# Kernel tuning notes

Hardware: AMD Instinct MI355X
Metric: run time of the kernel (lower is better)

The kernel has to match this reference:

```python
import jax, jax.numpy as jnp
import numpy as np

B, T, D, F = 32, 512, 512, 256
K = 3
MEL_MAX = 4096
EPS = 1e-5


def _xavier(key, shape, fan_in, fan_out):
    lim = float(np.sqrt(6.0 / (fan_in + fan_out)))
    return jax.random.uniform(key, shape, jnp.float32, -lim, lim)


def setup_inputs() -> dict:
    key = jax.random.key(0)
    ks = jax.random.split(key, 6)
    x = jax.random.normal(ks[0], (B, T, D), jnp.float32)
    target = jax.random.randint(ks[1], (B, T), 0, 8)  # per-token durations
    # conv weights stored as [K, I, O] (lax 'WIO'); torch xavier on [O,I,K]: fan_in=I*K, fan_out=O*K
    w1 = _xavier(ks[2], (K, D, F), D * K, F * K)
    b1 = jnp.zeros((F,), jnp.float32)
    g1 = jnp.ones((F,), jnp.float32)
    be1 = jnp.zeros((F,), jnp.float32)
    w2 = _xavier(ks[3], (K, F, F), F * K, F * K)
    b2 = jnp.zeros((F,), jnp.float32)
    g2 = jnp.ones((F,), jnp.float32)
    be2 = jnp.zeros((F,), jnp.float32)
    wl = _xavier(ks[4], (F, 1), F, 1)
    bl = jnp.zeros((1,), jnp.float32)
    return dict(x=x, target=target, mel_max_length=MEL_MAX,
                w1=w1, b1=b1, g1=g1, be1=be1,
                w2=w2, b2=b2, g2=g2, be2=be2, wl=wl, bl=bl)


def _layer_norm(h, g, b):
    mu = jnp.mean(h, axis=-1, keepdims=True)
    var = jnp.mean(jnp.square(h - mu), axis=-1, keepdims=True)
    return (h - mu) * jax.lax.rsqrt(var + EPS) * g + b


def _conv1d(h, w, b):
    # h: [B,T,C_in], w: [K,C_in,C_out]; torch padding=1 with K=3 == SAME
    out = jax.lax.conv_general_dilated(h, w, (1,), 'SAME',
                                       dimension_numbers=('NWC', 'WIO', 'NWC'))
    return out + b


def reference(x, target, mel_max_length, w1, b1, g1, be1, w2, b2, g2, be2, wl, bl):
    # ---- DurationPredictor (eval: dropout = identity) ----
    h = jax.nn.relu(_layer_norm(_conv1d(x, w1, b1), g1, be1))
    h = jax.nn.relu(_layer_norm(_conv1d(h, w2, b2), g2, be2))
    dur_pred = jax.nn.relu(h @ wl + bl)[..., 0]  # [B, T]

    # ---- LR: ragged expansion of x by `target` durations, padded to mel_max_length ----
    cum = jnp.cumsum(target, axis=1)              # [B, T]
    total = cum[:, -1]                            # [B]
    pos = jnp.arange(mel_max_length)              # [M]
    # frame m maps to token i with cum[i-1] <= m < cum[i]
    idx = jax.vmap(lambda c: jnp.searchsorted(c, pos, side='right'))(cum)  # [B, M]
    idx = jnp.clip(idx, 0, x.shape[1] - 1)
    mask = pos[None, :] < total[:, None]          # [B, M]
    out = jnp.take_along_axis(x, idx[..., None], axis=1) * mask[..., None].astype(x.dtype)
    return (out, dur_pred)
```

## Files before the change

### kernel.cpp

```cpp
#include <hip/hip_runtime.h>
#include <type_traits>

#define B_   32
#define T_   512
#define D_   512
#define F_   256
#define MEL  4096
#define EPS_ 1e-5f

typedef __attribute__((ext_vector_type(8))) short bf16x8;
typedef __attribute__((ext_vector_type(4))) float f32x4;

#define GLL16(gp, lp) \
    __builtin_amdgcn_global_load_lds((const __attribute__((address_space(1))) void*)(gp), \
                                     (__attribute__((address_space(3))) void*)(lp), 16, 0, 0)
#define BARRIER() do { asm volatile("" ::: "memory"); __builtin_amdgcn_s_barrier(); \
                       asm volatile("" ::: "memory"); } while (0)

__device__ inline unsigned short f2bf(float f) {
    unsigned u = __float_as_uint(f);
    unsigned r = (u + 0x7fff + ((u >> 16) & 1)) >> 16;
    return (unsigned short)r;
}

__global__ void prep_w_kernel(const float* __restrict__ w1, const float* __restrict__ w2,
                              unsigned short* __restrict__ w1T, unsigned short* __restrict__ w2T)
{
    int idx = blockIdx.x * 256 + threadIdx.x;
    if (idx < 3 * D_ * F_) {
        int kk = idx / F_, f = idx % F_;
        w1T[(size_t)f * (3 * D_) + kk] = f2bf(w1[idx]);
    } else {
        int j = idx - 3 * D_ * F_;
        if (j < 3 * F_ * F_) {
            int kk = j / F_, f = j % F_;
            w2T[(size_t)f * (3 * F_) + kk] = f2bf(w2[j]);
        }
    }
}

template<int IN_D, typename InT, bool FUSE_DUR>
__global__ __launch_bounds__(512, 1)
void conv_mfma_kernel(const InT* __restrict__ x, const unsigned short* __restrict__ wT,
                      const float* __restrict__ bias, const float* __restrict__ gamma,
                      const float* __restrict__ beta, unsigned short* __restrict__ out,
                      const float* __restrict__ wl, const float* __restrict__ bl,
                      float* __restrict__ dur)
{
    constexpr int MT = 64;
    constexpr int KT = 3 * IN_D;
    constexpr int PHASES = KT / 64;

    __shared__ __align__(16) char xs_raw[(MT + 2) * IN_D * 2];
    __shared__ __align__(16) unsigned short xsB[2 * 16384];
    __shared__ float red[MT][8];
    __shared__ float redD[MT][4];

    const int blocksPerBatch = T_ / MT;
    const int b  = blockIdx.x / blocksPerBatch;
    const int t0 = (blockIdx.x % blocksPerBatch) * MT;
    const int l  = threadIdx.x & 63;
    const int wv = threadIdx.x >> 6;
    const int fg = wv & 3;
    const int rg = wv >> 2;

    constexpr int CH = (MT + 2) * IN_D / 8;
    for (int c = threadIdx.x; c < CH; c += 512) {
        int j  = c / (IN_D / 8);
        int d8 = (c % (IN_D / 8)) * 8;
        int t  = t0 - 1 + j;
        uint4 pk = make_uint4(0u, 0u, 0u, 0u);
        if (t >= 0 && t < T_) {
            if constexpr (std::is_same_v<InT, float>) {
                const float4* src = reinterpret_cast<const float4*>(&x[((size_t)b * T_ + t) * IN_D + d8]);
                float4 a0 = src[0], a1 = src[1];
                pk.x = (unsigned)f2bf(a0.x) | ((unsigned)f2bf(a0.y) << 16);
                pk.y = (unsigned)f2bf(a0.z) | ((unsigned)f2bf(a0.w) << 16);
                pk.z = (unsigned)f2bf(a1.x) | ((unsigned)f2bf(a1.y) << 16);
                pk.w = (unsigned)f2bf(a1.z) | ((unsigned)f2bf(a1.w) << 16);
            } else {
                pk = *reinterpret_cast<const uint4*>(&x[((size_t)b * T_ + t) * IN_D + d8]);
            }
        }
        int byte = ((j * IN_D + d8) * 2) ^ ((j & 7) << 4);
        *reinterpret_cast<uint4*>(&xs_raw[byte]) = pk;
    }

    float bv[4], gv[4], bev[4], wlv[4];
#pragma unroll
    for (int n = 0; n < 4; ++n) {
        int f = fg * 64 + n * 16 + (l & 15);
        bv[n] = bias[f]; gv[n] = gamma[f]; bev[n] = beta[f];
        if constexpr (FUSE_DUR) wlv[n] = wl[f];
    }
    float blv = FUSE_DUR ? bl[0] : 0.f;

    __syncthreads();

    const int sbase = wv * 4;
    auto stageB = [&](int ph, int buf) {
        int p = ph < PHASES ? ph : PHASES - 1;
        unsigned short* lb = &xsB[buf * 16384];
#pragma unroll
        for (int i = 0; i < 4; ++i) {
            int s = sbase + i;
            int c = s * 64 + l;
            int f = c >> 3;
            int kg = (c & 7) ^ (f & 7);
            const unsigned short* src = wT + (size_t)f * KT + p * 64 + kg * 8;
            GLL16(src, lb + s * 512);
        }
    };

    auto loadBfrag = [&](bf16x8* dst, int buf, int kk2) {
#pragma unroll
        for (int n = 0; n < 4; ++n) {
            int f  = fg * 64 + n * 16 + (l & 15);
            int kg = kk2 * 4 + (l >> 4);
            dst[n] = *reinterpret_cast<const bf16x8*>(&xsB[buf * 16384 + f * 64 + ((kg ^ (f & 7)) * 8)]);
        }
    };
    const int k_lane = (l >> 4) * 8;
    auto loadA = [&](bf16x8* dst, int kk) {
        int kp = kk / IN_D;
        int dbase = (kk % IN_D) + k_lane;
#pragma unroll
        for (int m = 0; m < 2; ++m) {
            int j = rg * 32 + m * 16 + (l & 15) + kp;
            int byte = ((j * IN_D + dbase) * 2) ^ ((j & 7) << 4);
            dst[m] = *reinterpret_cast<const bf16x8*>(&xs_raw[byte]);
        }
    };

    f32x4 acc[2][4];
#pragma unroll
    for (int m = 0; m < 2; ++m)
#pragma unroll
        for (int n = 0; n < 4; ++n) acc[m][n] = (f32x4){0.f, 0.f, 0.f, 0.f};

    stageB(0, 0);
    stageB(1, 1);
    for (int p = 0; p < PHASES; ++p) {
        asm volatile("s_waitcnt vmcnt(4)" ::: "memory");
        BARRIER();
        int buf = p & 1;
#pragma unroll
        for (int kk2 = 0; kk2 < 2; ++kk2) {
            int kk = p * 64 + kk2 * 32;
            bf16x8 Bv[4], Av[2];
            loadBfrag(Bv, buf, kk2);
            loadA(Av, kk);
#pragma unroll
            for (int m = 0; m < 2; ++m)
#pragma unroll
                for (int n = 0; n < 4; ++n)
                    acc[m][n] = __builtin_amdgcn_mfma_f32_16x16x32_bf16(Av[m], Bv[n], acc[m][n], 0, 0, 0);
        }
        BARRIER();
        stageB(p + 2, buf);
    }

#pragma unroll
    for (int m = 0; m < 2; ++m)
#pragma unroll
        for (int q = 0; q < 4; ++q) {
            float s = 0.f, s2 = 0.f;
#pragma unroll
            for (int n = 0; n < 4; ++n) {
                float v = acc[m][n][q] + bv[n];
                acc[m][n][q] = v;
                s += v; s2 += v * v;
            }
#pragma unroll
            for (int o = 1; o < 16; o <<= 1) { s += __shfl_xor(s, o); s2 += __shfl_xor(s2, o); }
            int row = rg * 32 + m * 16 + (l >> 4) * 4 + q;
            if ((l & 15) == 0) { red[row][fg * 2] = s; red[row][fg * 2 + 1] = s2; }
        }
    __syncthreads();

#pragma unroll
    for (int m = 0; m < 2; ++m)
#pragma unroll
        for (int q = 0; q < 4; ++q) {
            int row = rg * 32 + m * 16 + (l >> 4) * 4 + q;
            float s  = red[row][0] + red[row][2] + red[row][4] + red[row][6];
            float s2 = red[row][1] + red[row][3] + red[row][5] + red[row][7];
            float mu  = s * (1.f / F_);
            float var = s2 * (1.f / F_) - mu * mu;
            float rs  = rsqrtf(var + EPS_);
            size_t rbase = ((size_t)(b * T_ + t0 + row)) * F_;
            float part = 0.f;
#pragma unroll
            for (int n = 0; n < 4; ++n) {
                float y = (acc[m][n][q] - mu) * rs * gv[n] + bev[n];
                y = fmaxf(y, 0.f);
                out[rbase + fg * 64 + n * 16 + (l & 15)] = f2bf(y);
                if constexpr (FUSE_DUR) part = fmaf(y, wlv[n], part);
            }
            if constexpr (FUSE_DUR) {
#pragma unroll
                for (int o = 1; o < 16; o <<= 1) part += __shfl_xor(part, o);
                if ((l & 15) == 0) redD[row][fg] = part;
            }
        }

    if constexpr (FUSE_DUR) {
        __syncthreads();
        if (threadIdx.x < MT) {
            float s = redD[threadIdx.x][0] + redD[threadIdx.x][1]
                    + redD[threadIdx.x][2] + redD[threadIdx.x][3] + blv;
            dur[(size_t)b * T_ + t0 + threadIdx.x] = fmaxf(s, 0.f);
        }
    }
}

__global__ __launch_bounds__(256)
void cumsum_kernel(const int* __restrict__ tgt, int* __restrict__ cum)
{
    int b = blockIdx.x;
    int tid = threadIdx.x;
    int t0 = tid * 2;
    int a0 = tgt[b * T_ + t0], a1 = tgt[b * T_ + t0 + 1];
    int lane = tid & 63, w = tid >> 6;
    int v = a0 + a1;
#pragma unroll
    for (int o = 1; o < 64; o <<= 1) { int u = __shfl_up(v, o); if (lane >= o) v += u; }
    __shared__ int wsum[4];
    if (lane == 63) wsum[w] = v;
    __syncthreads();
    int base = 0;
#pragma unroll
    for (int i = 0; i < 4; ++i) if (i < w) base += wsum[i];
    int incl = base + v;
    cum[b * T_ + t0]     = incl - a1;
    cum[b * T_ + t0 + 1] = incl;
}

__global__ __launch_bounds__(256)
void gather_kernel(const float* __restrict__ x, const int* __restrict__ cum,
                   float* __restrict__ out)
{
    int lane = threadIdx.x & 63, wid = threadIdx.x >> 6;
    int r = blockIdx.x * 4 + wid;
    int b   = r >> 12;
    int pos = r & (MEL - 1);
    const int* c = cum + b * T_;
    int total = c[T_ - 1];

    float4 v0 = make_float4(0.f, 0.f, 0.f, 0.f), v1 = v0;
    if (pos < total) {
        int lo = 0, hi = T_;
        while (lo < hi) { int mid = (lo + hi) >> 1; if (c[mid] <= pos) lo = mid + 1; else hi = mid; }
        int idx = min(lo, T_ - 1);
        const float* src = x + ((size_t)b * T_ + idx) * D_ + lane * 8;
        v0 = *reinterpret_cast<const float4*>(src);
        v1 = *reinterpret_cast<const float4*>(src + 4);
    }
    float* dst = out + (size_t)r * D_ + lane * 8;
    *reinterpret_cast<float4*>(dst)     = v0;
    *reinterpret_cast<float4*>(dst + 4) = v1;
}

extern "C" void kernel_launch(void* const* d_in, const int* in_sizes, int n_in,
                              void* d_out, int out_size, void* d_ws, size_t ws_size,
                              hipStream_t stream)
{
    const float* x      = (const float*)d_in[0];
    const int*   target = (const int*)d_in[1];
    const float* w1  = (const float*)d_in[3];
    const float* b1  = (const float*)d_in[4];
    const float* g1  = (const float*)d_in[5];
    const float* be1 = (const float*)d_in[6];
    const float* w2  = (const float*)d_in[7];
    const float* b2  = (const float*)d_in[8];
    const float* g2  = (const float*)d_in[9];
    const float* be2 = (const float*)d_in[10];
    const float* wl  = (const float*)d_in[11];
    const float* bl  = (const float*)d_in[12];

    float* out = (float*)d_out;
    float* dur = out + (size_t)B_ * MEL * D_;

    char* ws = (char*)d_ws;
    unsigned short* w1T = (unsigned short*)ws;         ws += (size_t)F_ * (3 * D_) * 2;
    unsigned short* w2T = (unsigned short*)ws;         ws += (size_t)F_ * (3 * F_) * 2;
    unsigned short* h1  = (unsigned short*)ws;         ws += (size_t)B_ * T_ * F_ * 2;
    unsigned short* h2  = (unsigned short*)ws;         ws += (size_t)B_ * T_ * F_ * 2;
    int*            cum = (int*)ws;

    const int prepN = 3 * D_ * F_ + 3 * F_ * F_;
    prep_w_kernel<<<(prepN + 255) / 256, 256, 0, stream>>>(w1, w2, w1T, w2T);

    conv_mfma_kernel<D_, float, false><<<B_ * (T_ / 64), 512, 0, stream>>>(
        x, w1T, b1, g1, be1, h1, nullptr, nullptr, nullptr);
    conv_mfma_kernel<F_, unsigned short, true><<<B_ * (T_ / 64), 512, 0, stream>>>(
        h1, w2T, b2, g2, be2, h2, wl, bl, dur);

    cumsum_kernel<<<B_, 256, 0, stream>>>(target, cum);
    gather_kernel<<<(B_ * MEL) / 4, 256, 0, stream>>>(x, cum, out);
}
```

Measured before the change: 113.0 us.

## Overlap ragged gather with conv kernels via extra warps and precompute indices

```diff
diff --git a/kernel.cpp b/kernel.cpp
--- a/kernel.cpp
+++ b/kernel.cpp
@@ -23,43 +23,109 @@
     return (unsigned short)r;
 }
 
-__global__ void prep_w_kernel(const float* __restrict__ w1, const float* __restrict__ w2,
-                              unsigned short* __restrict__ w1T, unsigned short* __restrict__ w2T)
+#define PREP_WBLOCKS 2304
+
+__global__ __launch_bounds__(256)
+void prep_kernel(const float* __restrict__ w1, const float* __restrict__ w2,
+                 const int* __restrict__ tgt,
+                 unsigned short* __restrict__ w1T, unsigned short* __restrict__ w2T,
+                 int* __restrict__ gidx)
 {
-    int idx = blockIdx.x * 256 + threadIdx.x;
-    if (idx < 3 * D_ * F_) {
-        int kk = idx / F_, f = idx % F_;
-        w1T[(size_t)f * (3 * D_) + kk] = f2bf(w1[idx]);
-    } else {
-        int j = idx - 3 * D_ * F_;
-        if (j < 3 * F_ * F_) {
+    __shared__ int lcum[T_];
+    __shared__ int wsum[4];
+
+    int bid = blockIdx.x;
+    int tid = threadIdx.x;
+    if (bid < PREP_WBLOCKS) {
+        int idx = bid * 256 + tid;
+        if (idx < 3 * D_ * F_) {
+            int kk = idx / F_, f = idx % F_;
+            w1T[(size_t)f * (3 * D_) + kk] = f2bf(w1[idx]);
+        } else {
+            int j = idx - 3 * D_ * F_;
             int kk = j / F_, f = j % F_;
             w2T[(size_t)f * (3 * F_) + kk] = f2bf(w2[j]);
         }
+        return;
+    }
+
+    int b = bid - PREP_WBLOCKS;
+    int t0 = tid * 2;
+    int a0 = tgt[b * T_ + t0], a1 = tgt[b * T_ + t0 + 1];
+    int lane = tid & 63, w = tid >> 6;
+    int v = a0 + a1;
+#pragma unroll
+    for (int o = 1; o < 64; o <<= 1) { int u = __shfl_up(v, o); if (lane >= o) v += u; }
+    if (lane == 63) wsum[w] = v;
+    __syncthreads();
+    int base = 0;
+#pragma unroll
+    for (int i = 0; i < 4; ++i) if (i < w) base += wsum[i];
+    int incl = base + v;
+    lcum[t0]     = incl - a1;
+    lcum[t0 + 1] = incl;
+    __syncthreads();
+
+    int total = lcum[T_ - 1];
+#pragma unroll
+    for (int k = 0; k < MEL / 256; ++k) {
+        int pos = tid + k * 256;
+        int lo = 0, hi = T_;
+        while (lo < hi) { int mid = (lo + hi) >> 1; if (lcum[mid] <= pos) lo = mid + 1; else hi = mid; }
+        gidx[b * MEL + pos] = (pos < total) ? min(lo, T_ - 1) : -1;
     }
 }
 
-template<int IN_D, typename InT, bool FUSE_DUR>
-__global__ __launch_bounds__(512, 1)
-void conv_mfma_kernel(const InT* __restrict__ x, const unsigned short* __restrict__ wT,
-                      const float* __restrict__ bias, const float* __restrict__ gamma,
-                      const float* __restrict__ beta, unsigned short* __restrict__ out,
-                      const float* __restrict__ wl, const float* __restrict__ bl,
-                      float* __restrict__ dur)
+template<int IN_D, typename InT, bool FUSE_DUR, int GROWS, int GOFF>
+__global__ __launch_bounds__(1024)
+void conv_gather_kernel(const InT* __restrict__ x, const unsigned short* __restrict__ wT,
+                        const float* __restrict__ bias, const float* __restrict__ gamma,
+                        const float* __restrict__ beta, unsigned short* __restrict__ out,
+                        const float* __restrict__ wl, const float* __restrict__ bl,
+                        float* __restrict__ dur,
+                        const float* __restrict__ xf, const int* __restrict__ gidx,
+                        float* __restrict__ gout)
 {
     constexpr int MT = 64;
     constexpr int KT = 3 * IN_D;
     constexpr int PHASES = KT / 64;
+    constexpr int NBAR = 2 + 2 * PHASES + (FUSE_DUR ? 1 : 0);
 
     __shared__ __align__(16) char xs_raw[(MT + 2) * IN_D * 2];
     __shared__ __align__(16) unsigned short xsB[2 * 16384];
     __shared__ float red[MT][8];
     __shared__ float redD[MT][4];
 
+    const int l = threadIdx.x & 63;
+
+    if (threadIdx.x >= 512) {
+        const int gw = (threadIdx.x >> 6) - 8;
+        const int rbase = GOFF + blockIdx.x * (GROWS * 8) + gw * GROWS;
+        int myidx = (l < GROWS) ? gidx[rbase + l] : -1;
+        int done = 0;
+        for (int bar = 0; bar < NBAR; ++bar) {
+            __builtin_amdgcn_s_barrier();
+            int tgt = (int)(((long)(bar + 1) * GROWS) / NBAR);
+            for (; done < tgt; ++done) {
+                int r = rbase + done;
+                int ix = __shfl(myidx, done);
+                float4 v0 = make_float4(0.f, 0.f, 0.f, 0.f), v1 = v0;
+                if (ix >= 0) {
+                    const float* s = xf + ((size_t)(r >> 12) * T_ + ix) * D_ + l * 8;
+                    v0 = *reinterpret_cast<const float4*>(s);
+                    v1 = *reinterpret_cast<const float4*>(s + 4);
+                }
+                float* d = gout + (size_t)r * D_ + l * 8;
+                *reinterpret_cast<float4*>(d)     = v0;
+                *reinterpret_cast<float4*>(d + 4) = v1;
+            }
+        }
+        return;
+    }
+
     const int blocksPerBatch = T_ / MT;
     const int b  = blockIdx.x / blocksPerBatch;
     const int t0 = (blockIdx.x % blocksPerBatch) * MT;
-    const int l  = threadIdx.x & 63;
     const int wv = threadIdx.x >> 6;
     const int fg = wv & 3;
     const int rg = wv >> 2;
@@ -111,7 +177,6 @@
             GLL16(src, lb + s * 512);
         }
     };
-
     auto loadBfrag = [&](bf16x8* dst, int buf, int kk2) {
 #pragma unroll
         for (int n = 0; n < 4; ++n) {
@@ -167,9 +232,9 @@
             float s = 0.f, s2 = 0.f;
 #pragma unroll
             for (int n = 0; n < 4; ++n) {
-                float v = acc[m][n][q] + bv[n];
-                acc[m][n][q] = v;
-                s += v; s2 += v * v;
+                float v2 = acc[m][n][q] + bv[n];
+                acc[m][n][q] = v2;
+                s += v2; s2 += v2 * v2;
             }
 #pragma unroll
             for (int o = 1; o < 16; o <<= 1) { s += __shfl_xor(s, o); s2 += __shfl_xor(s2, o); }
@@ -212,53 +277,6 @@
             dur[(size_t)b * T_ + t0 + threadIdx.x] = fmaxf(s, 0.f);
         }
     }
-}
-
-__global__ __launch_bounds__(256)
-void cumsum_kernel(const int* __restrict__ tgt, int* __restrict__ cum)
-{
-    int b = blockIdx.x;
-    int tid = threadIdx.x;
-    int t0 = tid * 2;
-    int a0 = tgt[b * T_ + t0], a1 = tgt[b * T_ + t0 + 1];
-    int lane = tid & 63, w = tid >> 6;
-    int v = a0 + a1;
-#pragma unroll
-    for (int o = 1; o < 64; o <<= 1) { int u = __shfl_up(v, o); if (lane >= o) v += u; }
-    __shared__ int wsum[4];
-    if (lane == 63) wsum[w] = v;
-    __syncthreads();
-    int base = 0;
-#pragma unroll
-    for (int i = 0; i < 4; ++i) if (i < w) base += wsum[i];
-    int incl = base + v;
-    cum[b * T_ + t0]     = incl - a1;
-    cum[b * T_ + t0 + 1] = incl;
-}
-
-__global__ __launch_bounds__(256)
-void gather_kernel(const float* __restrict__ x, const int* __restrict__ cum,
-                   float* __restrict__ out)
-{
-    int lane = threadIdx.x & 63, wid = threadIdx.x >> 6;
-    int r = blockIdx.x * 4 + wid;
-    int b   = r >> 12;
-    int pos = r & (MEL - 1);
-    const int* c = cum + b * T_;
-    int total = c[T_ - 1];
-
-    float4 v0 = make_float4(0.f, 0.f, 0.f, 0.f), v1 = v0;
-    if (pos < total) {
-        int lo = 0, hi = T_;
-        while (lo < hi) { int mid = (lo + hi) >> 1; if (c[mid] <= pos) lo = mid + 1; else hi = mid; }
-        int idx = min(lo, T_ - 1);
-        const float* src = x + ((size_t)b * T_ + idx) * D_ + lane * 8;
-        v0 = *reinterpret_cast<const float4*>(src);
-        v1 = *reinterpret_cast<const float4*>(src + 4);
-    }
-    float* dst = out + (size_t)r * D_ + lane * 8;
-    *reinterpret_cast<float4*>(dst)     = v0;
-    *reinterpret_cast<float4*>(dst + 4) = v1;
 }
 
 extern "C" void kernel_launch(void* const* d_in, const int* in_sizes, int n_in,
@@ -286,16 +304,12 @@
     unsigned short* w2T = (unsigned short*)ws;         ws += (size_t)F_ * (3 * F_) * 2;
     unsigned short* h1  = (unsigned short*)ws;         ws += (size_t)B_ * T_ * F_ * 2;
     unsigned short* h2  = (unsigned short*)ws;         ws += (size_t)B_ * T_ * F_ * 2;
-    int*            cum = (int*)ws;
-
-    const int prepN = 3 * D_ * F_ + 3 * F_ * F_;
-    prep_w_kernel<<<(prepN + 255) / 256, 256, 0, stream>>>(w1, w2, w1T, w2T);
-
-    conv_mfma_kernel<D_, float, false><<<B_ * (T_ / 64), 512, 0, stream>>>(
-        x, w1T, b1, g1, be1, h1, nullptr, nullptr, nullptr);
-    conv_mfma_kernel<F_, unsigned short, true><<<B_ * (T_ / 64), 512, 0, stream>>>(
-        h1, w2T, b2, g2, be2, h2, wl, bl, dur);
-
-    cumsum_kernel<<<B_, 256, 0, stream>>>(target, cum);
-    gather_kernel<<<(B_ * MEL) / 4, 256, 0, stream>>>(x, cum, out);
+    int*            gidx = (int*)ws;
+
+    prep_kernel<<<PREP_WBLOCKS + B_, 256, 0, stream>>>(w1, w2, target, w1T, w2T, gidx);
+
+    conv_gather_kernel<D_, float, false, 40, 0><<<B_ * (T_ / 64), 1024, 0, stream>>>(
+        x, w1T, b1, g1, be1, h1, nullptr, nullptr, nullptr, x, gidx, out);
+    conv_gather_kernel<F_, unsigned short, true, 24, 81920><<<B_ * (T_ / 64), 1024, 0, stream>>>(
+        h1, w2T, b2, g2, be2, h2, wl, bl, dur, x, gidx, out);
 }
```

After: 108.6 us. -3.9%, faster.
